# Optimization experiments

Measured on AMD Instinct MI355X. Metric: run time of the kernel, lower is better.

Reference implementation:

```python
import jax, jax.numpy as jnp
import numpy as np
from jax import lax

D_MODEL = 768
D_STATE = 16
D_CONV = 4
EXPAND = 2
D_INNER = EXPAND * D_MODEL  # 1536
DT_RANK = (D_MODEL + 15) // 16  # 48
BATCH = 4
SEQ_LEN = 2048


def setup_inputs() -> dict:
    key = jax.random.key(0)
    ks = jax.random.split(key, 8)
    x = jax.random.normal(ks[0], (BATCH, SEQ_LEN, D_MODEL), dtype=jnp.float32)
    W_in = jax.random.normal(ks[1], (D_INNER * 2, D_MODEL), dtype=jnp.float32) * 0.02
    conv_w = jax.random.normal(ks[2], (D_INNER, 1, D_CONV), dtype=jnp.float32) * 0.1
    conv_b = jnp.zeros((D_INNER,), dtype=jnp.float32)
    W_x = jax.random.normal(ks[3], (DT_RANK + 2 * D_STATE, D_INNER), dtype=jnp.float32) * 0.02
    dt_std = DT_RANK ** -0.5
    W_dt = jax.random.uniform(ks[4], (D_INNER, DT_RANK), minval=-dt_std, maxval=dt_std, dtype=jnp.float32)
    b_dt = jnp.zeros((D_INNER,), dtype=jnp.float32)
    A_log = jnp.log(jnp.tile(jnp.arange(1, D_STATE + 1, dtype=jnp.float32), (D_INNER, 1)))
    D_param = jnp.ones((D_INNER,), dtype=jnp.float32)
    W_out = jax.random.normal(ks[5], (D_MODEL, D_INNER), dtype=jnp.float32) * 0.02
    return {"x": x, "W_in": W_in, "conv_w": conv_w, "conv_b": conv_b,
            "W_x": W_x, "W_dt": W_dt, "b_dt": b_dt, "A_log": A_log,
            "D_param": D_param, "W_out": W_out}


def _silu(v):
    return v * jax.nn.sigmoid(v)


def reference(x, W_in, conv_w, conv_b, W_x, W_dt, b_dt, A_log, D_param, W_out):
    B, L, _ = x.shape
    # in_proj and split into x-branch / gate z
    xz = jnp.einsum('bld,ed->ble', x, W_in)            # (B, L, 2*d_inner)
    xb, z = jnp.split(xz, 2, axis=-1)
    # depthwise causal conv1d (torch pads both sides then truncates to L)
    xc = jnp.transpose(xb, (0, 2, 1))                   # (B, d_inner, L)
    xc = lax.conv_general_dilated(xc, conv_w, window_strides=(1,),
                                  padding=[(D_CONV - 1, 0)],
                                  feature_group_count=D_INNER,
                                  dimension_numbers=('NCH', 'OIH', 'NCH'))
    xc = xc + conv_b[None, :, None]
    xc = jnp.transpose(xc, (0, 2, 1))                   # (B, L, d_inner)
    xc = _silu(xc)
    # ssm input-dependent params
    x_dbl = jnp.einsum('bld,ed->ble', xc, W_x)          # (B, L, dt_rank+2*d_state)
    dt_r = x_dbl[..., :DT_RANK]
    Bm = x_dbl[..., DT_RANK:DT_RANK + D_STATE]          # (B, L, d_state)
    Cm = x_dbl[..., DT_RANK + D_STATE:]
    dt = jax.nn.softplus(jnp.einsum('blr,dr->bld', dt_r, W_dt) + b_dt)
    A = -jnp.exp(A_log)                                 # (d_inner, d_state)
    # selective scan over time
    def step(h, inp):
        x_t, dt_t, B_t, C_t = inp                       # (B,d_inner),(B,d_inner),(B,d_state),(B,d_state)
        dA = jnp.exp(dt_t[..., None] * A)               # (B, d_inner, d_state)
        h = dA * h + (dt_t * x_t)[..., None] * B_t[:, None, :]
        y_t = jnp.einsum('bdn,bn->bd', h, C_t) + D_param * x_t
        return h, y_t
    h0 = jnp.zeros((B, D_INNER, D_STATE), dtype=x.dtype)
    xs = (jnp.transpose(xc, (1, 0, 2)), jnp.transpose(dt, (1, 0, 2)),
          jnp.transpose(Bm, (1, 0, 2)), jnp.transpose(Cm, (1, 0, 2)))
    _, ys = lax.scan(step, h0, xs)                      # (L, B, d_inner)
    y = jnp.transpose(ys, (1, 0, 2))
    y = y * _silu(z)
    return jnp.einsum('bld,od->blo', y, W_out)
```

## Files before the change

kernel.cpp:

```cpp
#include <hip/hip_runtime.h>
#include <hip/hip_bf16.h>
#include <math.h>

#define D_MODEL   768
#define D_STATE   16
#define D_CONV    4
#define D_INNER   1536
#define DT_RANK   48
#define BATCH     4
#define SEQ_LEN   2048
#define BL        (BATCH * SEQ_LEN)
#define NCHUNK    32
#define CHUNK     (SEQ_LEN / NCHUNK)

typedef __bf16 bf16x8 __attribute__((ext_vector_type(8)));
typedef float  f32x4  __attribute__((ext_vector_type(4)));

__device__ __forceinline__ void async_copy16(const void* g, void* l) {
    __builtin_amdgcn_global_load_lds(
        (const __attribute__((address_space(1))) void*)g,
        (__attribute__((address_space(3))) void*)l,
        16, 0, 0);
}

template <int EPI>
__global__ __launch_bounds__(256)
void gemm_in(const __bf16* __restrict__ A, const __bf16* __restrict__ B,
             float* __restrict__ C, const float* __restrict__ bias,
             int M, int N, int K, int ldc)
{
    __shared__ __bf16 Asl[128 * 64];
    __shared__ __bf16 Bsl[128 * 64];

    const int tid  = threadIdx.x;
    const int lane = tid & 63;
    const int w    = tid >> 6;
    const int wm   = (w >> 1) * 64;
    const int wn   = (w & 1) * 64;

    const int bm = blockIdx.y * 128;
    const int bn = blockIdx.x * 128;

    const long lda = 2L * K;
    const long ldb = 2L * K;

    f32x4 acc[4][4];
    #pragma unroll
    for (int i = 0; i < 4; ++i)
        #pragma unroll
        for (int j = 0; j < 4; ++j)
            acc[i][j] = (f32x4){0.f, 0.f, 0.f, 0.f};

    const int srow = w * 32 + (lane >> 3);
    const int kc8  = ((lane & 7) ^ ((lane >> 3) & 7)) * 8;
    const __bf16* Abase = A + (long)(bm + srow) * lda + kc8;
    const __bf16* Bbase = B + (long)(bn + srow) * ldb + kc8;
    char* AslW = (char*)Asl + (w * 32) * 128;
    char* BslW = (char*)Bsl + (w * 32) * 128;

    const int fr = lane & 15;
    const int g4 = lane >> 4;
    const long lda8 = 8 * lda, ldb8 = 8 * ldb;

    const int aoff[3] = {0, 0, K};
    const int boff[3] = {0, K, 0};

    #pragma unroll
    for (int s = 0; s < 3; ++s) {
        const __bf16* Ab = Abase + aoff[s];
        const __bf16* Bb = Bbase + boff[s];
        for (int kk = 0; kk < K; kk += 64) {
            __syncthreads();
            #pragma unroll
            for (int j = 0; j < 4; ++j) {
                async_copy16(Ab + j * lda8 + kk, AslW + j * 1024);
                async_copy16(Bb + j * ldb8 + kk, BslW + j * 1024);
            }
            __syncthreads();

            #pragma unroll
            for (int ks = 0; ks < 2; ++ks) {
                const int c = ks * 4 + g4;
                bf16x8 af[4], bfr[4];
                #pragma unroll
                for (int t = 0; t < 4; ++t) {
                    const int ra = wm + t * 16 + fr;
                    const int rb = wn + t * 16 + fr;
                    af[t]  = *(const bf16x8*)&Asl[ra * 64 + ((c ^ (ra & 7)) * 8)];
                    bfr[t] = *(const bf16x8*)&Bsl[rb * 64 + ((c ^ (rb & 7)) * 8)];
                }
                #pragma unroll
                for (int i = 0; i < 4; ++i)
                    #pragma unroll
                    for (int j = 0; j < 4; ++j)
                        acc[i][j] = __builtin_amdgcn_mfma_f32_16x16x32_bf16(af[i], bfr[j], acc[i][j], 0, 0, 0);
            }
        }
    }

    const int cn  = lane & 15;
    const int cr4 = (lane >> 4) * 4;
    #pragma unroll
    for (int i = 0; i < 4; ++i)
        #pragma unroll
        for (int j = 0; j < 4; ++j)
            #pragma unroll
            for (int r = 0; r < 4; ++r) {
                const int row = bm + wm + i * 16 + cr4 + r;
                const int col = bn + wn + j * 16 + cn;
                float v = acc[i][j][r];
                if (EPI == 1) {
                    v += bias[col];
                    v = fmaxf(v, 0.f) + log1pf(__expf(-fabsf(v)));
                }
                C[(long)row * ldc + col] = v;
            }
}

__global__ __launch_bounds__(256)
void gemm_xdbl(const __bf16* __restrict__ A, const __bf16* __restrict__ B,
               float* __restrict__ Pout)
{
    __shared__ __bf16 Asl[128 * 32];
    __shared__ __bf16 Bsl[128 * 32];

    const int tid  = threadIdx.x;
    const int lane = tid & 63;
    const int w    = tid >> 6;
    const int wm   = (w >> 1) * 64;
    const int wn   = (w & 1) * 64;

    const int s  = blockIdx.x;
    const int bm = blockIdx.y * 128;
    const long lda = 3072, ldb = 3072;
    const int K = 1536;

    f32x4 acc[4][4];
    #pragma unroll
    for (int i = 0; i < 4; ++i)
        #pragma unroll
        for (int j = 0; j < 4; ++j)
            acc[i][j] = (f32x4){0.f, 0.f, 0.f, 0.f};

    const int srow = w * 32 + (lane >> 2);
    const int kc8  = (((lane & 3) ^ ((lane >> 2) & 3))) * 8;
    const __bf16* Abase = A + (long)(bm + srow) * lda + kc8;
    const __bf16* Bbase = B + (long)srow * ldb + kc8;
    char* AslW = (char*)Asl + (w * 32) * 64;
    char* BslW = (char*)Bsl + (w * 32) * 64;

    const int rdK = (((lane >> 4) ^ (lane & 3))) * 8;
    const int fr  = lane & 15;
    const long lda16 = 16 * lda, ldb16 = 16 * ldb;

    const int aoff[3] = {0, 0, K};
    const int boff[3] = {0, K, 0};
    const int kt0 = s * 36, kt1 = kt0 + 36;

    #pragma unroll
    for (int seg = 0; seg < 3; ++seg) {
        const int lo  = (kt0 > seg * 48)      ? kt0 : seg * 48;
        const int hiE = (kt1 < seg * 48 + 48) ? kt1 : seg * 48 + 48;
        const __bf16* Ab = Abase + aoff[seg];
        const __bf16* Bb = Bbase + boff[seg];
        for (int kt = lo; kt < hiE; ++kt) {
            const int kk = (kt - seg * 48) * 32;
            __syncthreads();
            async_copy16(Ab + kk,         AslW);
            async_copy16(Ab + lda16 + kk, AslW + 16 * 64);
            async_copy16(Bb + kk,         BslW);
            async_copy16(Bb + ldb16 + kk, BslW + 16 * 64);
            __syncthreads();

            bf16x8 af[4], bfr[4];
            #pragma unroll
            for (int t = 0; t < 4; ++t) {
                af[t]  = *(const bf16x8*)&Asl[(wm + t * 16 + fr) * 32 + rdK];
                bfr[t] = *(const bf16x8*)&Bsl[(wn + t * 16 + fr) * 32 + rdK];
            }
            #pragma unroll
            for (int i = 0; i < 4; ++i)
                #pragma unroll
                for (int j = 0; j < 4; ++j)
                    acc[i][j] = __builtin_amdgcn_mfma_f32_16x16x32_bf16(af[i], bfr[j], acc[i][j], 0, 0, 0);
        }
    }

    float* Cp = Pout + (long)s * (8192L * 128);
    const int cn  = lane & 15;
    const int cr4 = (lane >> 4) * 4;
    #pragma unroll
    for (int i = 0; i < 4; ++i)
        #pragma unroll
        for (int j = 0; j < 4; ++j)
            #pragma unroll
            for (int r = 0; r < 4; ++r) {
                const int row = bm + wm + i * 16 + cr4 + r;
                const int col = wn + j * 16 + cn;
                Cp[(long)row * 128 + col] = acc[i][j][r];
            }
}

__global__ __launch_bounds__(256)
void xdbl_reduce3(const float* __restrict__ Pout, float* __restrict__ xbc,
                  __bf16* __restrict__ xdtS)
{
    const long i = (long)blockIdx.x * 256 + threadIdx.x;
    if (i >= 8192L * 128) return;
    const long r  = i >> 7;
    const int  c  = (int)(i & 127);
    const long st = 8192L * 128;
    const long rb = r * 128;

    const int k = c & 63;
    float u = 0.f;
    if (k < 48) {
        const long o = rb + k;
        u = (Pout[o] + Pout[o + st]) + (Pout[o + 2 * st] + Pout[o + 3 * st]);
    }
    const __bf16 hi = (__bf16)u;
    xdtS[rb + c] = (c < 64) ? hi : (__bf16)(u - (float)hi);

    if (c >= 96) {
        const int j = c - 96;
        const long o = rb + 48 + j;
        xbc[r * 32 + j] =
            (Pout[o] + Pout[o + st]) + (Pout[o + 2 * st] + Pout[o + 3 * st]);
    }
}

#define NW0 ((long)BL * 768)
#define NW1 (3072L * 768)
#define NW2 (768L * 1536)
#define NW3 (80L * 1536)
#define NW4 (1536L * 128)
__global__ __launch_bounds__(256)
void split_all(const float* __restrict__ x,
               const float* __restrict__ W_in, const float* __restrict__ W_out,
               const float* __restrict__ W_x, const float* __restrict__ W_dt,
               __bf16* __restrict__ xS,
               __bf16* __restrict__ wInS, __bf16* __restrict__ wOutS,
               __bf16* __restrict__ wXS, __bf16* __restrict__ wDtS)
{
    long i = (long)blockIdx.x * 256 + threadIdx.x;
    if (i < NW0) {
        const long row = i / 768; const int col = (int)(i - row * 768);
        const float a = x[i];
        const __bf16 h = (__bf16)a;
        __bf16* d = xS + row * 1536 + col;
        d[0] = h; d[768] = (__bf16)(a - (float)h);
        return;
    }
    i -= NW0;
    if (i < NW1) {
        const long row = i / 768; const int col = (int)(i - row * 768);
        const float a = W_in[i];
        const __bf16 h = (__bf16)a;
        __bf16* d = wInS + row * 1536 + col;
        d[0] = h; d[768] = (__bf16)(a - (float)h);
        return;
    }
    i -= NW1;
    if (i < NW2) {
        const long row = i / 1536; const int col = (int)(i - row * 1536);
        const float a = W_out[i];
        const __bf16 h = (__bf16)a;
        __bf16* d = wOutS + row * 3072 + col;
        d[0] = h; d[1536] = (__bf16)(a - (float)h);
        return;
    }
    i -= NW2;
    if (i < NW3) {
        const long row = i / 1536; const int col = (int)(i - row * 1536);
        const float a = W_x[i];
        const __bf16 h = (__bf16)a;
        __bf16* d = wXS + row * 3072 + col;
        d[0] = h; d[1536] = (__bf16)(a - (float)h);
        return;
    }
    i -= NW3;
    if (i < NW4) {
        const long row = i >> 7; const int c = (int)(i & 127);
        const int k = c & 63;
        const float a = (k < 48) ? W_dt[row * 48 + k] : 0.f;
        const __bf16 h = (__bf16)a;
        wDtS[row * 128 + c] = (c < 64) ? h : (__bf16)(a - (float)h);
    }
}

__global__ __launch_bounds__(256)
void conv_silu_kernel(const float* __restrict__ xz,
                      const float* __restrict__ conv_w,
                      const float* __restrict__ conv_b,
                      __bf16* __restrict__ xcS)
{
    const long idx = (long)blockIdx.x * 256 + threadIdx.x;
    const int d  = (int)(idx % D_INNER);
    const long bl = idx / D_INNER;
    const int l  = (int)(bl % SEQ_LEN);

    const float w0 = conv_w[d * 4 + 0];
    const float w1 = conv_w[d * 4 + 1];
    const float w2 = conv_w[d * 4 + 2];
    const float w3 = conv_w[d * 4 + 3];

    const float* base = xz + bl * 3072 + d;
    float s = conv_b[d];
    if (l >= 3) s = fmaf(base[-3 * 3072], w0, s);
    if (l >= 2) s = fmaf(base[-2 * 3072], w1, s);
    if (l >= 1) s = fmaf(base[-1 * 3072], w2, s);
    s = fmaf(base[0], w3, s);
    const float sig = 1.f / (1.f + __expf(-s));
    const float v = s * sig;
    const __bf16 hi = (__bf16)v;
    const __bf16 lo = (__bf16)(v - (float)hi);
    xcS[bl * 3072 + d]        = hi;
    xcS[bl * 3072 + 1536 + d] = lo;
}

__global__ __launch_bounds__(256)
void scan_phaseA(const __bf16* __restrict__ xcS, const float* __restrict__ xz,
                 const float* __restrict__ xbc, const float* __restrict__ A_log,
                 float* __restrict__ P, float* __restrict__ S)
{
    const int d = blockIdx.x * 256 + threadIdx.x;
    const int c = blockIdx.y;
    const int b = blockIdx.z;

    float An[16], Pr[16], Sr[16];
    #pragma unroll
    for (int n = 0; n < 16; ++n) {
        An[n] = -__expf(A_log[d * 16 + n]);
        Pr[n] = 1.f;
        Sr[n] = 0.f;
    }

    const long bl0 = (long)b * SEQ_LEN + (long)c * CHUNK;
    for (int l = 0; l < CHUNK; ++l) {
        const long bl = bl0 + l;
        const float dt  = xz[bl * 3072 + d];
        const float x   = (float)xcS[bl * 3072 + d] + (float)xcS[bl * 3072 + 1536 + d];
        const float dtx = dt * x;
        const float* bc = xbc + bl * 32;
        #pragma unroll
        for (int n = 0; n < 16; ++n) {
            const float a = __expf(dt * An[n]);
            Pr[n] *= a;
            Sr[n] = fmaf(a, Sr[n], dtx * bc[n]);
        }
    }

    const long base = ((long)(b * NCHUNK + c) * 16) * D_INNER + d;
    #pragma unroll
    for (int n = 0; n < 16; ++n) {
        P[base + (long)n * D_INNER] = Pr[n];
        S[base + (long)n * D_INNER] = Sr[n];
    }
}

__global__ __launch_bounds__(256)
void scan_phaseB(const float* __restrict__ P, const float* __restrict__ S,
                 float* __restrict__ H)
{
    const int t = blockIdx.x * 256 + threadIdx.x;
    const int d = t % D_INNER;
    const int r = t / D_INNER;
    const int n = r & 15;
    const int b = r >> 4;

    float h = 0.f;
    for (int c = 0; c < NCHUNK; ++c) {
        const long i = ((long)(b * NCHUNK + c) * 16 + n) * D_INNER + d;
        H[i] = h;
        h = fmaf(P[i], h, S[i]);
    }
}

__global__ __launch_bounds__(256)
void scan_phaseC(__bf16* xcS_yS, const float* __restrict__ xz,
                 const float* __restrict__ xbc, const float* __restrict__ A_log,
                 const float* __restrict__ Dp, const float* __restrict__ H)
{
    const int d = blockIdx.x * 256 + threadIdx.x;
    const int c = blockIdx.y;
    const int b = blockIdx.z;

    float An[16], h[16];
    const long hbase = ((long)(b * NCHUNK + c) * 16) * D_INNER + d;
    #pragma unroll
    for (int n = 0; n < 16; ++n) {
        An[n] = -__expf(A_log[d * 16 + n]);
        h[n]  = H[hbase + (long)n * D_INNER];
    }
    const float Dd = Dp[d];

    const long bl0 = (long)b * SEQ_LEN + (long)c * CHUNK;
    for (int l = 0; l < CHUNK; ++l) {
        const long bl = bl0 + l;
        const float dt  = xz[bl * 3072 + d];
        const float x   = (float)xcS_yS[bl * 3072 + d] + (float)xcS_yS[bl * 3072 + 1536 + d];
        const float dtx = dt * x;
        const float* bc = xbc + bl * 32;
        float y = Dd * x;
        #pragma unroll
        for (int n = 0; n < 16; ++n) {
            const float a = __expf(dt * An[n]);
            h[n] = fmaf(a, h[n], dtx * bc[n]);
            y = fmaf(h[n], bc[16 + n], y);
        }
        const float z  = xz[bl * 3072 + D_INNER + d];
        const float sz = z / (1.f + __expf(-z));
        const float v  = y * sz;
        const __bf16 hi = (__bf16)v;
        const __bf16 lo = (__bf16)(v - (float)hi);
        xcS_yS[bl * 3072 + d]        = hi;
        xcS_yS[bl * 3072 + 1536 + d] = lo;
    }
}

extern "C" void kernel_launch(void* const* d_in, const int* in_sizes, int n_in,
                              void* d_out, int out_size, void* d_ws, size_t ws_size,
                              hipStream_t stream)
{
    const float* x      = (const float*)d_in[0];
    const float* W_in   = (const float*)d_in[1];
    const float* conv_w = (const float*)d_in[2];
    const float* conv_b = (const float*)d_in[3];
    const float* W_x    = (const float*)d_in[4];
    const float* W_dt   = (const float*)d_in[5];
    const float* b_dt   = (const float*)d_in[6];
    const float* A_log  = (const float*)d_in[7];
    const float* D_p    = (const float*)d_in[8];
    const float* W_out  = (const float*)d_in[9];
    float* out = (float*)d_out;

    char* p = (char*)d_ws;
    auto take = [&](size_t bytes) { char* r = p; p += (bytes + 255) & ~(size_t)255; return r; };

    float*  xz    = (float*)take((size_t)BL * 3072 * 4);
    float*  H     = (float*)take((size_t)BATCH * NCHUNK * 16 * D_INNER * 4);
    __bf16* wOutS = (__bf16*)take(768L * 3072 * 2);
    __bf16* wXS   = (__bf16*)take(128L * 3072 * 2);
    __bf16* wDtS  = (__bf16*)take(1536L * 128 * 2);
    __bf16* xdtS  = (__bf16*)take(8192L * 128 * 2);
    float*  xbc   = (float*)take(8192L * 32 * 4);
    float*  Pout  = (float*)take(4L * 8192 * 128 * 4);
    float*  S     = (float*)take((size_t)BATCH * NCHUNK * 16 * D_INNER * 4);
    float*  P     = Pout;

    char* region = take(50331648);
    __bf16* xS   = (__bf16*)region;
    __bf16* wInS = (__bf16*)(region + 25165824);
    __bf16* xcS  = (__bf16*)region;
    __bf16* yS   = (__bf16*)region;

    {
        const long n = NW0 + NW1 + NW2 + NW3 + NW4;
        split_all<<<(int)((n + 255) / 256), 256, 0, stream>>>(
            x, W_in, W_out, W_x, W_dt, xS, wInS, wOutS, wXS, wDtS);
    }
    {
        dim3 grid(3072 / 128, BL / 128);
        gemm_in<0><<<grid, 256, 0, stream>>>(xS, wInS, xz, nullptr,
                                             BL, 3072, 768, 3072);
    }
    {
        const long total = (long)BL * D_INNER;
        conv_silu_kernel<<<(int)(total / 256), 256, 0, stream>>>(xz, conv_w, conv_b, xcS);
    }
    {
        dim3 grid(4, BL / 128);
        gemm_xdbl<<<grid, 256, 0, stream>>>(xcS, wXS, Pout);
    }
    {
        const long n = 8192L * 128;
        xdbl_reduce3<<<(int)((n + 255) / 256), 256, 0, stream>>>(Pout, xbc, xdtS);
    }
    {
        dim3 grid(1536 / 128, BL / 128);
        gemm_in<1><<<grid, 256, 0, stream>>>(xdtS, wDtS, xz, b_dt,
                                             BL, 1536, 64, 3072);
    }
    {
        dim3 grid(D_INNER / 256, NCHUNK, BATCH);
        scan_phaseA<<<grid, 256, 0, stream>>>(xcS, xz, xbc, A_log, P, S);
    }
    scan_phaseB<<<(BATCH * 16 * D_INNER) / 256, 256, 0, stream>>>(P, S, H);
    {
        dim3 grid(D_INNER / 256, NCHUNK, BATCH);
        scan_phaseC<<<grid, 256, 0, stream>>>(xcS, xz, xbc, A_log, D_p, H);
    }
    {
        dim3 grid(768 / 128, BL / 128);
        gemm_in<0><<<grid, 256, 0, stream>>>(yS, wOutS, out, nullptr,
                                             BL, 768, 1536, 768);
    }
}
```

Measured before the change: 571.9 us.

## Fuse split-bf16 hi/lo passes into a single K loop per GEMM tile

The GEMMs emulate fp32 with split bf16 (hi/lo) operands. Previously they made three separate passes over K (hi*hi, hi*lo, lo*hi), loading tiles again for each pass. Now each 64-wide LDS row holds 32 hi and 32 lo elements, so one K loop loads both halves and issues all three MFMAs per fragment. This cuts global loads and barrier count by about a third. The cost is more register use for four fragment sets and a different layout of LDS reads.

```diff
diff --git a/kernel.cpp b/kernel.cpp
--- a/kernel.cpp
+++ b/kernel.cpp
@@ -25,9 +25,9 @@
 
 template <int EPI>
 __global__ __launch_bounds__(256)
-void gemm_in(const __bf16* __restrict__ A, const __bf16* __restrict__ B,
-             float* __restrict__ C, const float* __restrict__ bias,
-             int M, int N, int K, int ldc)
+void gemm_f(const __bf16* __restrict__ A, const __bf16* __restrict__ B,
+            float* __restrict__ C, const float* __restrict__ bias,
+            int M, int N, int K, int ldc)
 {
     __shared__ __bf16 Asl[128 * 64];
     __shared__ __bf16 Bsl[128 * 64];
@@ -52,9 +52,10 @@
             acc[i][j] = (f32x4){0.f, 0.f, 0.f, 0.f};
 
     const int srow = w * 32 + (lane >> 3);
-    const int kc8  = ((lane & 7) ^ ((lane >> 3) & 7)) * 8;
-    const __bf16* Abase = A + (long)(bm + srow) * lda + kc8;
-    const __bf16* Bbase = B + (long)(bn + srow) * ldb + kc8;
+    const int q    = (lane & 7) ^ ((lane >> 3) & 7);
+    const int qoff = (q < 4) ? q * 8 : K + (q - 4) * 8;
+    const __bf16* Abase = A + (long)(bm + srow) * lda + qoff;
+    const __bf16* Bbase = B + (long)(bn + srow) * ldb + qoff;
     char* AslW = (char*)Asl + (w * 32) * 128;
     char* BslW = (char*)Bsl + (w * 32) * 128;
 
@@ -62,40 +63,33 @@
     const int g4 = lane >> 4;
     const long lda8 = 8 * lda, ldb8 = 8 * ldb;
 
-    const int aoff[3] = {0, 0, K};
-    const int boff[3] = {0, K, 0};
-
-    #pragma unroll
-    for (int s = 0; s < 3; ++s) {
-        const __bf16* Ab = Abase + aoff[s];
-        const __bf16* Bb = Bbase + boff[s];
-        for (int kk = 0; kk < K; kk += 64) {
-            __syncthreads();
+    for (int kk = 0; kk < K; kk += 32) {
+        __syncthreads();
+        #pragma unroll
+        for (int j = 0; j < 4; ++j) {
+            async_copy16(Abase + j * lda8 + kk, AslW + j * 1024);
+            async_copy16(Bbase + j * ldb8 + kk, BslW + j * 1024);
+        }
+        __syncthreads();
+
+        bf16x8 ah[4], al[4], bh[4], bl[4];
+        #pragma unroll
+        for (int t = 0; t < 4; ++t) {
+            const int ra = wm + t * 16 + fr;
+            const int rb = wn + t * 16 + fr;
+            ah[t] = *(const bf16x8*)&Asl[ra * 64 + ((g4       ^ (ra & 7)) * 8)];
+            al[t] = *(const bf16x8*)&Asl[ra * 64 + (((4 + g4) ^ (ra & 7)) * 8)];
+            bh[t] = *(const bf16x8*)&Bsl[rb * 64 + ((g4       ^ (rb & 7)) * 8)];
+            bl[t] = *(const bf16x8*)&Bsl[rb * 64 + (((4 + g4) ^ (rb & 7)) * 8)];
+        }
+        #pragma unroll
+        for (int i = 0; i < 4; ++i)
             #pragma unroll
             for (int j = 0; j < 4; ++j) {
-                async_copy16(Ab + j * lda8 + kk, AslW + j * 1024);
-                async_copy16(Bb + j * ldb8 + kk, BslW + j * 1024);
+                acc[i][j] = __builtin_amdgcn_mfma_f32_16x16x32_bf16(ah[i], bh[j], acc[i][j], 0, 0, 0);
+                acc[i][j] = __builtin_amdgcn_mfma_f32_16x16x32_bf16(ah[i], bl[j], acc[i][j], 0, 0, 0);
+                acc[i][j] = __builtin_amdgcn_mfma_f32_16x16x32_bf16(al[i], bh[j], acc[i][j], 0, 0, 0);
             }
-            __syncthreads();
-
-            #pragma unroll
-            for (int ks = 0; ks < 2; ++ks) {
-                const int c = ks * 4 + g4;
-                bf16x8 af[4], bfr[4];
-                #pragma unroll
-                for (int t = 0; t < 4; ++t) {
-                    const int ra = wm + t * 16 + fr;
-                    const int rb = wn + t * 16 + fr;
-                    af[t]  = *(const bf16x8*)&Asl[ra * 64 + ((c ^ (ra & 7)) * 8)];
-                    bfr[t] = *(const bf16x8*)&Bsl[rb * 64 + ((c ^ (rb & 7)) * 8)];
-                }
-                #pragma unroll
-                for (int i = 0; i < 4; ++i)
-                    #pragma unroll
-                    for (int j = 0; j < 4; ++j)
-                        acc[i][j] = __builtin_amdgcn_mfma_f32_16x16x32_bf16(af[i], bfr[j], acc[i][j], 0, 0, 0);
-            }
-        }
     }
 
     const int cn  = lane & 15;
@@ -121,8 +115,8 @@
 void gemm_xdbl(const __bf16* __restrict__ A, const __bf16* __restrict__ B,
                float* __restrict__ Pout)
 {
-    __shared__ __bf16 Asl[128 * 32];
-    __shared__ __bf16 Bsl[128 * 32];
+    __shared__ __bf16 Asl[128 * 64];
+    __shared__ __bf16 Bsl[128 * 64];
 
     const int tid  = threadIdx.x;
     const int lane = tid & 63;
@@ -132,8 +126,8 @@
 
     const int s  = blockIdx.x;
     const int bm = blockIdx.y * 128;
+    const int K  = 1536;
     const long lda = 3072, ldb = 3072;
-    const int K = 1536;
 
     f32x4 acc[4][4];
     #pragma unroll
@@ -142,48 +136,46 @@
         for (int j = 0; j < 4; ++j)
             acc[i][j] = (f32x4){0.f, 0.f, 0.f, 0.f};
 
-    const int srow = w * 32 + (lane >> 2);
-    const int kc8  = (((lane & 3) ^ ((lane >> 2) & 3))) * 8;
-    const __bf16* Abase = A + (long)(bm + srow) * lda + kc8;
-    const __bf16* Bbase = B + (long)srow * ldb + kc8;
-    char* AslW = (char*)Asl + (w * 32) * 64;
-    char* BslW = (char*)Bsl + (w * 32) * 64;
-
-    const int rdK = (((lane >> 4) ^ (lane & 3))) * 8;
-    const int fr  = lane & 15;
-    const long lda16 = 16 * lda, ldb16 = 16 * ldb;
-
-    const int aoff[3] = {0, 0, K};
-    const int boff[3] = {0, K, 0};
-    const int kt0 = s * 36, kt1 = kt0 + 36;
-
-    #pragma unroll
-    for (int seg = 0; seg < 3; ++seg) {
-        const int lo  = (kt0 > seg * 48)      ? kt0 : seg * 48;
-        const int hiE = (kt1 < seg * 48 + 48) ? kt1 : seg * 48 + 48;
-        const __bf16* Ab = Abase + aoff[seg];
-        const __bf16* Bb = Bbase + boff[seg];
-        for (int kt = lo; kt < hiE; ++kt) {
-            const int kk = (kt - seg * 48) * 32;
-            __syncthreads();
-            async_copy16(Ab + kk,         AslW);
-            async_copy16(Ab + lda16 + kk, AslW + 16 * 64);
-            async_copy16(Bb + kk,         BslW);
-            async_copy16(Bb + ldb16 + kk, BslW + 16 * 64);
-            __syncthreads();
-
-            bf16x8 af[4], bfr[4];
+    const int srow = w * 32 + (lane >> 3);
+    const int q    = (lane & 7) ^ ((lane >> 3) & 7);
+    const int qoff = (q < 4) ? q * 8 : K + (q - 4) * 8;
+    const __bf16* Abase = A + (long)(bm + srow) * lda + qoff;
+    const __bf16* Bbase = B + (long)srow * ldb + qoff;
+    char* AslW = (char*)Asl + (w * 32) * 128;
+    char* BslW = (char*)Bsl + (w * 32) * 128;
+
+    const int fr = lane & 15;
+    const int g4 = lane >> 4;
+    const long lda8 = 8 * lda, ldb8 = 8 * ldb;
+
+    for (int kt = s * 12; kt < (s + 1) * 12; ++kt) {
+        const int kk = kt * 32;
+        __syncthreads();
+        #pragma unroll
+        for (int j = 0; j < 4; ++j) {
+            async_copy16(Abase + j * lda8 + kk, AslW + j * 1024);
+            async_copy16(Bbase + j * ldb8 + kk, BslW + j * 1024);
+        }
+        __syncthreads();
+
+        bf16x8 ah[4], al[4], bh[4], bl[4];
+        #pragma unroll
+        for (int t = 0; t < 4; ++t) {
+            const int ra = wm + t * 16 + fr;
+            const int rb = wn + t * 16 + fr;
+            ah[t] = *(const bf16x8*)&Asl[ra * 64 + ((g4       ^ (ra & 7)) * 8)];
+            al[t] = *(const bf16x8*)&Asl[ra * 64 + (((4 + g4) ^ (ra & 7)) * 8)];
+            bh[t] = *(const bf16x8*)&Bsl[rb * 64 + ((g4       ^ (rb & 7)) * 8)];
+            bl[t] = *(const bf16x8*)&Bsl[rb * 64 + (((4 + g4) ^ (rb & 7)) * 8)];
+        }
+        #pragma unroll
+        for (int i = 0; i < 4; ++i)
             #pragma unroll
-            for (int t = 0; t < 4; ++t) {
-                af[t]  = *(const bf16x8*)&Asl[(wm + t * 16 + fr) * 32 + rdK];
-                bfr[t] = *(const bf16x8*)&Bsl[(wn + t * 16 + fr) * 32 + rdK];
+            for (int j = 0; j < 4; ++j) {
+                acc[i][j] = __builtin_amdgcn_mfma_f32_16x16x32_bf16(ah[i], bh[j], acc[i][j], 0, 0, 0);
+                acc[i][j] = __builtin_amdgcn_mfma_f32_16x16x32_bf16(ah[i], bl[j], acc[i][j], 0, 0, 0);
+                acc[i][j] = __builtin_amdgcn_mfma_f32_16x16x32_bf16(al[i], bh[j], acc[i][j], 0, 0, 0);
             }
-            #pragma unroll
-            for (int i = 0; i < 4; ++i)
-                #pragma unroll
-                for (int j = 0; j < 4; ++j)
-                    acc[i][j] = __builtin_amdgcn_mfma_f32_16x16x32_bf16(af[i], bfr[j], acc[i][j], 0, 0, 0);
-        }
     }
 
     float* Cp = Pout + (long)s * (8192L * 128);
@@ -461,8 +453,8 @@
     }
     {
         dim3 grid(3072 / 128, BL / 128);
-        gemm_in<0><<<grid, 256, 0, stream>>>(xS, wInS, xz, nullptr,
-                                             BL, 3072, 768, 3072);
+        gemm_f<0><<<grid, 256, 0, stream>>>(xS, wInS, xz, nullptr,
+                                            BL, 3072, 768, 3072);
     }
     {
         const long total = (long)BL * D_INNER;
@@ -478,8 +470,8 @@
     }
     {
         dim3 grid(1536 / 128, BL / 128);
-        gemm_in<1><<<grid, 256, 0, stream>>>(xdtS, wDtS, xz, b_dt,
-                                             BL, 1536, 64, 3072);
+        gemm_f<1><<<grid, 256, 0, stream>>>(xdtS, wDtS, xz, b_dt,
+                                            BL, 1536, 64, 3072);
     }
     {
         dim3 grid(D_INNER / 256, NCHUNK, BATCH);
@@ -492,7 +484,7 @@
     }
     {
         dim3 grid(768 / 128, BL / 128);
-        gemm_in<0><<<grid, 256, 0, stream>>>(yS, wOutS, out, nullptr,
-                                             BL, 768, 1536, 768);
-    }
-}
+        gemm_f<0><<<grid, 256, 0, stream>>>(yS, wOutS, out, nullptr,
+                                            BL, 768, 1536, 768);
+    }
+}
```

After: 529.8 us. 1.08x faster.
